# Kernel tuning notes

Hardware: AMD Instinct MI355X
Metric: run time of the kernel (lower is better)

Reference implementation:

```python
import jax, jax.numpy as jnp
import numpy as np

B, S, D, H = 2, 2048, 1024, 16
DK = D // H

def setup_inputs() -> dict:
    key = jax.random.key(0)
    ks = jax.random.split(key, 9)
    sc = 1.0 / np.sqrt(D)
    return {
        "query": jax.random.normal(ks[0], (B, S, D), jnp.float32),
        "key_": jax.random.normal(ks[1], (B, S, D), jnp.float32),
        "value": jax.random.normal(ks[2], (B, S, D), jnp.float32),
        "Wq": jax.random.normal(ks[3], (D, D), jnp.float32) * sc,
        "bq": jnp.zeros((D,), jnp.float32),
        "Wk": jax.random.normal(ks[4], (D, D), jnp.float32) * sc,
        "bk": jnp.zeros((D,), jnp.float32),
        "Wv": jax.random.normal(ks[5], (D, D), jnp.float32) * sc,
        "bv": jnp.zeros((D,), jnp.float32),
    }

def reference(query, key_, value, Wq, bq, Wk, bk, Wv, bv):
    # QKV projections -> [B, H, S, DK]
    def heads(x, W, b):
        return (x @ W + b).reshape(B, S, H, DK).transpose(0, 2, 1, 3)
    q = heads(query, Wq, bq)
    k = heads(key_, Wk, bk)
    v = heads(value, Wv, bv)
    scores = jnp.einsum('bhsd,bhtd->bhst', q, k) / jnp.sqrt(jnp.float32(DK))
    attn = jax.nn.softmax(scores, axis=-1)  # dropout = identity (eval)
    ctx = jnp.einsum('bhst,bhtd->bhsd', attn, v)
    return ctx.transpose(0, 2, 1, 3).reshape(B, S, D)
```

## Files before the change

kernel.cpp:

```cpp
#include <hip/hip_runtime.h>
#include <hip/hip_bf16.h>

typedef __bf16 bf16x4 __attribute__((ext_vector_type(4)));
typedef __bf16 bf16x8 __attribute__((ext_vector_type(8)));
typedef float  f32x4  __attribute__((ext_vector_type(4)));
typedef float  f32x16 __attribute__((ext_vector_type(16)));

constexpr int B = 2, S = 2048, D = 1024, H = 16, DK = 64;
constexpr int M = B * S;
constexpr int BH = B * H;

__device__ inline float fexp2(float x) {
#if __has_builtin(__builtin_amdgcn_exp2f)
  return __builtin_amdgcn_exp2f(x);
#else
  return exp2f(x);
#endif
}
__device__ inline float frcp(float x) {
#if __has_builtin(__builtin_amdgcn_rcpf)
  return __builtin_amdgcn_rcpf(x);
#else
  return 1.0f / x;
#endif
}
__device__ inline unsigned pk2(float lo, float hi) {
  union { __bf16 h[2]; unsigned u; } x;
  x.h[0] = (__bf16)lo; x.h[1] = (__bf16)hi;
  return x.u;
}

__global__ __launch_bounds__(256) void wtrans3(const float* __restrict__ w0,
                                               const float* __restrict__ w1,
                                               const float* __restrict__ w2,
                                               __bf16* __restrict__ t0,
                                               __bf16* __restrict__ t1,
                                               __bf16* __restrict__ t2) {
  int z = blockIdx.z;
  const float* W = z == 0 ? w0 : z == 1 ? w1 : w2;
  __bf16* WT = z == 0 ? t0 : z == 1 ? t1 : t2;
  __shared__ float t[32][33];
  int tx = threadIdx.x & 31, ty0 = threadIdx.x >> 5;
  int n0 = blockIdx.x * 32, k0 = blockIdx.y * 32;
#pragma unroll
  for (int i = 0; i < 4; ++i)
    t[ty0 + i * 8][tx] = W[(size_t)(k0 + ty0 + i * 8) * D + n0 + tx];
  __syncthreads();
#pragma unroll
  for (int i = 0; i < 4; ++i)
    WT[(size_t)(n0 + ty0 + i * 8) * D + k0 + tx] = (__bf16)t[tx][ty0 + i * 8];
}

constexpr int TM = 128, TN = 128, BK = 64;

__global__ __launch_bounds__(256, 3) void proj3(
    const float* __restrict__ X0, const float* __restrict__ X1,
    const float* __restrict__ X2, const __bf16* __restrict__ W0,
    const __bf16* __restrict__ W1, const __bf16* __restrict__ W2,
    const float* __restrict__ b0, const float* __restrict__ b1,
    const float* __restrict__ b2, __bf16* __restrict__ Qo,
    __bf16* __restrict__ Ko, __bf16* __restrict__ Vo) {
  __shared__ __align__(16) __bf16 As[TM * BK];
  __shared__ __align__(16) __bf16 Bs[TN * BK];
  int z = blockIdx.z;
  const float* A   = z == 0 ? X0 : z == 1 ? X1 : X2;
  const __bf16* BT = z == 0 ? W0 : z == 1 ? W1 : W2;
  const float* bias = z == 0 ? b0 : z == 1 ? b1 : b2;
  __bf16* out = z == 0 ? Qo : z == 1 ? Ko : Vo;
  int mode = (z == 2) ? 1 : 0;
  float osc = (z == 0) ? 0.18033688011112042f : 1.0f;

  int t = threadIdx.x;
  int fid = blockIdx.x;
  int xcd = fid & 7, slot = fid >> 3;
  int m0 = (xcd * 4 + (slot >> 3)) * TM;
  int n0 = (slot & 7) * TN;
  int w = t >> 6, lane = t & 63, c = lane & 15, g = lane >> 4;
  int wr = w >> 1, wc = w & 1;

  f32x4 acc[4][4];
#pragma unroll
  for (int i = 0; i < 4; ++i)
#pragma unroll
    for (int j = 0; j < 4; ++j) acc[i][j] = f32x4{0.f, 0.f, 0.f, 0.f};

  int srcoff = (((t & 7) ^ ((t >> 3) & 7)) << 4);
  int srow = t >> 3;
  const float* aptr[4];
  const __bf16* bptr[4];
#pragma unroll
  for (int i = 0; i < 4; ++i) {
    aptr[i] = A + (size_t)(m0 + i * 32 + srow) * D + (srcoff >> 1);
    bptr[i] = BT + (size_t)(n0 + i * 32 + srow) * D + (srcoff >> 1);
  }

  float4 pa[4][2];
#pragma unroll
  for (int i = 0; i < 4; ++i) {
    pa[i][0] = *(const float4*)(aptr[i]);
    pa[i][1] = *(const float4*)(aptr[i] + 4);
  }

  int rswz = ((c & 7) << 4);

  for (int kk = 0; kk < D; kk += BK) {
#pragma unroll
    for (int i = 0; i < 4; ++i) {
      bf16x8 v;
      v[0] = (__bf16)pa[i][0].x; v[1] = (__bf16)pa[i][0].y;
      v[2] = (__bf16)pa[i][0].z; v[3] = (__bf16)pa[i][0].w;
      v[4] = (__bf16)pa[i][1].x; v[5] = (__bf16)pa[i][1].y;
      v[6] = (__bf16)pa[i][1].z; v[7] = (__bf16)pa[i][1].w;
      *(bf16x8*)((char*)As + i * 4096 + t * 16) = v;
    }
#pragma unroll
    for (int i = 0; i < 4; ++i)
      __builtin_amdgcn_global_load_lds(
          (const __attribute__((address_space(1))) unsigned int*)(bptr[i] + kk),
          (__attribute__((address_space(3))) unsigned int*)((char*)Bs + i * 4096 + t * 16), 16, 0, 0);
    __syncthreads();

    if (kk + BK < D) {
#pragma unroll
      for (int i = 0; i < 4; ++i) {
        pa[i][0] = *(const float4*)(aptr[i] + kk + BK);
        pa[i][1] = *(const float4*)(aptr[i] + kk + BK + 4);
      }
    }

#pragma unroll
    for (int ks = 0; ks < 2; ++ks) {
      int cb = (ks * 64 + g * 16) ^ rswz;
      bf16x8 af[4], bf[4];
#pragma unroll
      for (int i = 0; i < 4; ++i)
        af[i] = *(const bf16x8*)((char*)As + (wr * 64 + i * 16 + c) * 128 + cb);
#pragma unroll
      for (int j = 0; j < 4; ++j)
        bf[j] = *(const bf16x8*)((char*)Bs + (wc * 64 + j * 16 + c) * 128 + cb);
#pragma unroll
      for (int i = 0; i < 4; ++i)
#pragma unroll
        for (int j = 0; j < 4; ++j)
          acc[i][j] = __builtin_amdgcn_mfma_f32_16x16x32_bf16(af[i], bf[j], acc[i][j], 0, 0, 0);
    }
    __syncthreads();
  }

#pragma unroll
  for (int i = 0; i < 4; ++i)
#pragma unroll
    for (int j = 0; j < 4; ++j) {
      int n = n0 + wc * 64 + j * 16 + c;
      float bv = bias[n];
      int h = n >> 6, dk = n & 63;
#pragma unroll
      for (int q = 0; q < 4; ++q) {
        int mrow = m0 + wr * 64 + i * 16 + g * 4 + q;
        int b = mrow >> 11, s = mrow & (S - 1);
        float val = (acc[i][j][q] + bv) * osc;
        size_t idx;
        if (mode == 0) idx = ((size_t)(b * H + h) * S + s) * DK + dk;
        else           idx = ((size_t)(b * H + h) * DK + dk) * S + s;
        out[idx] = (__bf16)val;
      }
    }
}

constexpr int NSTEP = S / 128;

__global__ __launch_bounds__(256) void attn(const __bf16* __restrict__ Q,
                                            const __bf16* __restrict__ K,
                                            const __bf16* __restrict__ VT,
                                            float* __restrict__ out) {
  __shared__ __align__(16) __bf16 Ks[2][8192];
  __shared__ __align__(16) __bf16 Vs[2][8192];

  int t = threadIdx.x, w = t >> 6, lane = t & 63;
  int l31 = lane & 31, hi = lane >> 5;

  int fid = blockIdx.x;
  int xcd = fid & 7, slot = fid >> 3;
  int bh = xcd * 4 + (slot >> 4);
  int q0 = (slot & 15) * 128 + w * 32;

  const __bf16* Qb = Q + (size_t)bh * S * DK;
  const char* Kg = (const char*)(K + (size_t)bh * S * DK);
  const char* Vg = (const char*)(VT + (size_t)bh * DK * S);

  bf16x8 qf[4];
  {
    const __bf16* qp = Qb + (size_t)(q0 + l31) * DK + hi * 8;
#pragma unroll
    for (int s2 = 0; s2 < 4; ++s2) qf[s2] = *(const bf16x8*)(qp + s2 * 16);
  }

  f32x16 acc0, acc1;
#pragma unroll
  for (int r = 0; r < 16; ++r) { acc0[r] = 0.f; acc1[r] = 0.f; }
  float lrun = 0.f;

  int krow = ((l31 >> 2) & 1) * 8 + ((l31 >> 3) & 1) * 16 + ((l31 >> 4) & 1) * 4 + (l31 & 3);
  int kswz = (((krow & 7) ^ ((krow >> 3) & 3)) << 4);
  int vswz = (((l31 & 7) ^ ((l31 >> 3) & 3)) << 4);

  auto stage = [&](int bufi, int kstep) {
#pragma unroll
    for (int i = 0; i < 4; ++i) {
      int L = i * 4096 + t * 16;
      {
        int row = L >> 7;
        int sz = (((row & 7) ^ ((row >> 3) & 3)) << 4);
        __builtin_amdgcn_global_load_lds(
            (const __attribute__((address_space(1))) unsigned int*)(Kg + (size_t)kstep * 16384 + (L ^ sz)),
            (__attribute__((address_space(3))) unsigned int*)((char*)&Ks[bufi][0] + L), 16, 0, 0);
      }
      {
        int row = L >> 8;
        int sz = (((row & 7) ^ ((row >> 3) & 3)) << 4);
        __builtin_amdgcn_global_load_lds(
            (const __attribute__((address_space(1))) unsigned int*)(Vg + (size_t)row * (S * 2) + kstep * 256 + ((L & 255) ^ sz)),
            (__attribute__((address_space(3))) unsigned int*)((char*)&Vs[bufi][0] + L), 16, 0, 0);
      }
    }
  };

  stage(0, 0);
  __syncthreads();

  for (int tt = 0; tt < NSTEP; ++tt) {
    int cur = tt & 1;
    if (tt + 1 < NSTEP) stage(cur ^ 1, tt + 1);
    const char* kb = (const char*)&Ks[cur][0];
    const char* vb = (const char*)&Vs[cur][0];

#pragma unroll
    for (int sub = 0; sub < 4; ++sub) {
      bf16x8 Kf[4], Vf[4];
      {
        const char* kr = kb + ((sub * 32 + krow) << 7);
#pragma unroll
        for (int s2 = 0; s2 < 4; ++s2)
          Kf[s2] = *(const bf16x8*)(kr + ((s2 * 32 + hi * 16) ^ kswz));
      }
#pragma unroll
      for (int ks = 0; ks < 2; ++ks)
#pragma unroll
        for (int db = 0; db < 2; ++db)
          Vf[ks * 2 + db] = *(const bf16x8*)(vb + ((db * 32 + l31) << 8) +
                                             ((sub * 64 + ks * 32 + hi * 16) ^ vswz));

      f32x16 st;
#pragma unroll
      for (int r = 0; r < 16; ++r) st[r] = 0.f;
#pragma unroll
      for (int s2 = 0; s2 < 4; ++s2)
        st = __builtin_amdgcn_mfma_f32_32x32x16_bf16(Kf[s2], qf[s2], st, 0, 0, 0);

      float p[16];
#pragma unroll
      for (int r = 0; r < 16; ++r) p[r] = fexp2(st[r]);
      {
        float t0 = (p[0] + p[1]) + (p[2] + p[3]);
        float t1 = (p[4] + p[5]) + (p[6] + p[7]);
        float t2 = (p[8] + p[9]) + (p[10] + p[11]);
        float t3 = (p[12] + p[13]) + (p[14] + p[15]);
        lrun += (t0 + t1) + (t2 + t3);
      }

      union Pk { unsigned u[4]; bf16x8 v; } P0, P1;
      P0.u[0] = pk2(p[0], p[1]);   P0.u[1] = pk2(p[2], p[3]);
      P0.u[2] = pk2(p[8], p[9]);   P0.u[3] = pk2(p[10], p[11]);
      P1.u[0] = pk2(p[4], p[5]);   P1.u[1] = pk2(p[6], p[7]);
      P1.u[2] = pk2(p[12], p[13]); P1.u[3] = pk2(p[14], p[15]);

      acc0 = __builtin_amdgcn_mfma_f32_32x32x16_bf16(P0.v, Vf[0], acc0, 0, 0, 0);
      acc1 = __builtin_amdgcn_mfma_f32_32x32x16_bf16(P0.v, Vf[1], acc1, 0, 0, 0);
      acc0 = __builtin_amdgcn_mfma_f32_32x32x16_bf16(P1.v, Vf[2], acc0, 0, 0, 0);
      acc1 = __builtin_amdgcn_mfma_f32_32x32x16_bf16(P1.v, Vf[3], acc1, 0, 0, 0);
    }
    __syncthreads();
  }

  lrun += __shfl_xor(lrun, 32);
  int b = bh >> 4, h = bh & 15;
#pragma unroll
  for (int r = 0; r < 16; ++r) {
    int rowq = (r & 3) + 8 * (r >> 2) + 4 * hi;
    float li = __shfl(lrun, rowq);
    float ri = frcp(li);
    size_t base = (size_t)(b * S + q0 + rowq) * D + h * 64 + l31;
    out[base] = acc0[r] * ri;
    out[base + 32] = acc1[r] * ri;
  }
}

extern "C" void kernel_launch(void* const* d_in, const int* in_sizes, int n_in,
                              void* d_out, int out_size, void* d_ws, size_t ws_size,
                              hipStream_t stream) {
  (void)in_sizes; (void)n_in; (void)out_size; (void)ws_size;
  const float* xq = (const float*)d_in[0];
  const float* xk = (const float*)d_in[1];
  const float* xv = (const float*)d_in[2];
  const float* Wq = (const float*)d_in[3];
  const float* bq = (const float*)d_in[4];
  const float* Wk = (const float*)d_in[5];
  const float* bk = (const float*)d_in[6];
  const float* Wv = (const float*)d_in[7];
  const float* bv = (const float*)d_in[8];

  char* ws = (char*)d_ws;
  const size_t MB = 1u << 20;
  __bf16* WT[3] = {(__bf16*)(ws + 24 * MB), (__bf16*)(ws + 26 * MB), (__bf16*)(ws + 28 * MB)};
  __bf16* Qb = (__bf16*)(ws + 30 * MB);
  __bf16* Kb = (__bf16*)(ws + 38 * MB);
  __bf16* Vt = (__bf16*)(ws + 46 * MB);

  wtrans3<<<dim3(D / 32, D / 32, 3), 256, 0, stream>>>(Wq, Wk, Wv, WT[0], WT[1], WT[2]);
  proj3<<<dim3(256, 1, 3), 256, 0, stream>>>(xq, xk, xv,
                                             WT[0], WT[1], WT[2],
                                             bq, bk, bv, Qb, Kb, Vt);
  attn<<<dim3(512), 256, 0, stream>>>(Qb, Kb, Vt, (float*)d_out);
}
```

Before: 100.6 us.

## Double-buffer LDS fragment loads in attention loop and raise MFMA priority

Restructures the inner attention loop so LDS reads for the next sub-tile's K/V fragments are issued before computing the current one, using two register fragment sets. MFMA sections are wrapped in s_setprio to favour matrix issue, and launch bounds request two blocks per CU. The aim is to hide LDS latency behind MFMA work, at the cost of more live registers, which may conflict with the occupancy hint.

```diff
diff --git a/kernel.cpp b/kernel.cpp
--- a/kernel.cpp
+++ b/kernel.cpp
@@ -169,10 +169,10 @@
 
 constexpr int NSTEP = S / 128;
 
-__global__ __launch_bounds__(256) void attn(const __bf16* __restrict__ Q,
-                                            const __bf16* __restrict__ K,
-                                            const __bf16* __restrict__ VT,
-                                            float* __restrict__ out) {
+__global__ __launch_bounds__(256, 2) void attn(const __bf16* __restrict__ Q,
+                                               const __bf16* __restrict__ K,
+                                               const __bf16* __restrict__ VT,
+                                               float* __restrict__ out) {
   __shared__ __align__(16) __bf16 Ks[2][8192];
   __shared__ __align__(16) __bf16 Vs[2][8192];
 
@@ -194,6 +194,10 @@
 #pragma unroll
     for (int s2 = 0; s2 < 4; ++s2) qf[s2] = *(const bf16x8*)(qp + s2 * 16);
   }
+
+  f32x16 ZERO;
+#pragma unroll
+  for (int r = 0; r < 16; ++r) ZERO[r] = 0.f;
 
   f32x16 acc0, acc1;
 #pragma unroll
@@ -225,60 +229,71 @@
     }
   };
 
+  auto loadFrag = [&](const char* kb, const char* vb, int sub, bf16x8* Kf, bf16x8* Vf) {
+    const char* kr = kb + ((sub * 32 + krow) << 7);
+#pragma unroll
+    for (int s2 = 0; s2 < 4; ++s2)
+      Kf[s2] = *(const bf16x8*)(kr + ((s2 * 32 + hi * 16) ^ kswz));
+#pragma unroll
+    for (int ks = 0; ks < 2; ++ks)
+#pragma unroll
+      for (int db = 0; db < 2; ++db)
+        Vf[ks * 2 + db] = *(const bf16x8*)(vb + ((db * 32 + l31) << 8) +
+                                           ((sub * 64 + ks * 32 + hi * 16) ^ vswz));
+  };
+
+  auto computeSub = [&](bf16x8* Kf, bf16x8* Vf) {
+    __builtin_amdgcn_s_setprio(1);
+    f32x16 st = __builtin_amdgcn_mfma_f32_32x32x16_bf16(Kf[0], qf[0], ZERO, 0, 0, 0);
+    st = __builtin_amdgcn_mfma_f32_32x32x16_bf16(Kf[1], qf[1], st, 0, 0, 0);
+    st = __builtin_amdgcn_mfma_f32_32x32x16_bf16(Kf[2], qf[2], st, 0, 0, 0);
+    st = __builtin_amdgcn_mfma_f32_32x32x16_bf16(Kf[3], qf[3], st, 0, 0, 0);
+    __builtin_amdgcn_s_setprio(0);
+
+    float p[16];
+#pragma unroll
+    for (int r = 0; r < 16; ++r) p[r] = fexp2(st[r]);
+    {
+      float t0 = (p[0] + p[1]) + (p[2] + p[3]);
+      float t1 = (p[4] + p[5]) + (p[6] + p[7]);
+      float t2 = (p[8] + p[9]) + (p[10] + p[11]);
+      float t3 = (p[12] + p[13]) + (p[14] + p[15]);
+      lrun += (t0 + t1) + (t2 + t3);
+    }
+
+    union Pk { unsigned u[4]; bf16x8 v; } P0, P1;
+    P0.u[0] = pk2(p[0], p[1]);   P0.u[1] = pk2(p[2], p[3]);
+    P0.u[2] = pk2(p[8], p[9]);   P0.u[3] = pk2(p[10], p[11]);
+    P1.u[0] = pk2(p[4], p[5]);   P1.u[1] = pk2(p[6], p[7]);
+    P1.u[2] = pk2(p[12], p[13]); P1.u[3] = pk2(p[14], p[15]);
+
+    __builtin_amdgcn_s_setprio(1);
+    acc0 = __builtin_amdgcn_mfma_f32_32x32x16_bf16(P0.v, Vf[0], acc0, 0, 0, 0);
+    acc1 = __builtin_amdgcn_mfma_f32_32x32x16_bf16(P0.v, Vf[1], acc1, 0, 0, 0);
+    acc0 = __builtin_amdgcn_mfma_f32_32x32x16_bf16(P1.v, Vf[2], acc0, 0, 0, 0);
+    acc1 = __builtin_amdgcn_mfma_f32_32x32x16_bf16(P1.v, Vf[3], acc1, 0, 0, 0);
+    __builtin_amdgcn_s_setprio(0);
+  };
+
   stage(0, 0);
   __syncthreads();
 
+  bf16x8 KfA[4], VfA[4], KfB[4], VfB[4];
   for (int tt = 0; tt < NSTEP; ++tt) {
     int cur = tt & 1;
     if (tt + 1 < NSTEP) stage(cur ^ 1, tt + 1);
     const char* kb = (const char*)&Ks[cur][0];
     const char* vb = (const char*)&Vs[cur][0];
 
-#pragma unroll
-    for (int sub = 0; sub < 4; ++sub) {
-      bf16x8 Kf[4], Vf[4];
-      {
-        const char* kr = kb + ((sub * 32 + krow) << 7);
-#pragma unroll
-        for (int s2 = 0; s2 < 4; ++s2)
-          Kf[s2] = *(const bf16x8*)(kr + ((s2 * 32 + hi * 16) ^ kswz));
-      }
-#pragma unroll
-      for (int ks = 0; ks < 2; ++ks)
-#pragma unroll
-        for (int db = 0; db < 2; ++db)
-          Vf[ks * 2 + db] = *(const bf16x8*)(vb + ((db * 32 + l31) << 8) +
-                                             ((sub * 64 + ks * 32 + hi * 16) ^ vswz));
-
-      f32x16 st;
-#pragma unroll
-      for (int r = 0; r < 16; ++r) st[r] = 0.f;
-#pragma unroll
-      for (int s2 = 0; s2 < 4; ++s2)
-        st = __builtin_amdgcn_mfma_f32_32x32x16_bf16(Kf[s2], qf[s2], st, 0, 0, 0);
-
-      float p[16];
-#pragma unroll
-      for (int r = 0; r < 16; ++r) p[r] = fexp2(st[r]);
-      {
-        float t0 = (p[0] + p[1]) + (p[2] + p[3]);
-        float t1 = (p[4] + p[5]) + (p[6] + p[7]);
-        float t2 = (p[8] + p[9]) + (p[10] + p[11]);
-        float t3 = (p[12] + p[13]) + (p[14] + p[15]);
-        lrun += (t0 + t1) + (t2 + t3);
-      }
-
-      union Pk { unsigned u[4]; bf16x8 v; } P0, P1;
-      P0.u[0] = pk2(p[0], p[1]);   P0.u[1] = pk2(p[2], p[3]);
-      P0.u[2] = pk2(p[8], p[9]);   P0.u[3] = pk2(p[10], p[11]);
-      P1.u[0] = pk2(p[4], p[5]);   P1.u[1] = pk2(p[6], p[7]);
-      P1.u[2] = pk2(p[12], p[13]); P1.u[3] = pk2(p[14], p[15]);
-
-      acc0 = __builtin_amdgcn_mfma_f32_32x32x16_bf16(P0.v, Vf[0], acc0, 0, 0, 0);
-      acc1 = __builtin_amdgcn_mfma_f32_32x32x16_bf16(P0.v, Vf[1], acc1, 0, 0, 0);
-      acc0 = __builtin_amdgcn_mfma_f32_32x32x16_bf16(P1.v, Vf[2], acc0, 0, 0, 0);
-      acc1 = __builtin_amdgcn_mfma_f32_32x32x16_bf16(P1.v, Vf[3], acc1, 0, 0, 0);
-    }
+    loadFrag(kb, vb, 0, KfA, VfA);
+    loadFrag(kb, vb, 1, KfB, VfB);
+    computeSub(KfA, VfA);
+    loadFrag(kb, vb, 2, KfA, VfA);
+    computeSub(KfB, VfB);
+    loadFrag(kb, vb, 3, KfB, VfB);
+    computeSub(KfA, VfA);
+    computeSub(KfB, VfB);
+
     __syncthreads();
   }
 
```

Result: faster. 96.58 us (-4.0%).
